# Optimization experiments

Measured on AMD Instinct MI355X. Metric: run time of the kernel, lower is better.

Reference implementation:

```python
import jax, jax.numpy as jnp
import numpy as np

B, T, F, D, H, L, DFF, G = 4, 2048, 512, 1024, 16, 2, 4096, 16
WSCALE = 0.03  # ~1/sqrt(D) so activations stay well-conditioned


def setup_inputs() -> dict:
    key = jax.random.key(0)
    ks = iter(jax.random.split(key, 24))

    def w(shape):
        return jax.random.normal(next(ks), shape, jnp.float32) * WSCALE

    return {
        "x": jax.random.normal(next(ks), (B, T, F), jnp.float32),
        "proj_w": w((D, F)), "proj_b": jnp.zeros((D,), jnp.float32),
        "wq": w((L, D, D)), "wk": w((L, D, D)), "wv": w((L, D, D)),
        "bq": jnp.zeros((L, D), jnp.float32), "bk": jnp.zeros((L, D), jnp.float32), "bv": jnp.zeros((L, D), jnp.float32),
        "wo": w((L, D, D)), "bo": jnp.zeros((L, D), jnp.float32),
        "ln1_g": jnp.ones((L, D), jnp.float32), "ln1_b": jnp.zeros((L, D), jnp.float32),
        "ln2_g": jnp.ones((L, D), jnp.float32), "ln2_b": jnp.zeros((L, D), jnp.float32),
        "w1": w((L, DFF, D)), "b1": jnp.zeros((L, DFF), jnp.float32),
        "w2": w((L, D, DFF)), "b2": jnp.zeros((L, D), jnp.float32),
        "hw1": w((G, D, D)), "hb1": jnp.zeros((G, D), jnp.float32),
        "hw2": w((G, 2, D)), "hb2": jnp.zeros((G, 2), jnp.float32),
        "nhead": H,
    }


def _ln(x, g, b, eps=1e-5):
    m = x.mean(-1, keepdims=True)
    v = ((x - m) ** 2).mean(-1, keepdims=True)
    return (x - m) * jax.lax.rsqrt(v + eps) * g + b


def _pe(t, d):
    # sinusoidal positional encoding, shape (t, d) (d even -> sin/cos interleave)
    pos = jnp.arange(t, dtype=jnp.float32)[:, None]
    div = jnp.exp(jnp.arange(0, d, 2, dtype=jnp.float32) * (-np.log(10000.0) / d))
    ph = pos * div
    return jnp.stack([jnp.sin(ph), jnp.cos(ph)], axis=-1).reshape(t, d)


def reference(x, proj_w, proj_b, wq, wk, wv, bq, bk, bv, wo, bo,
              ln1_g, ln1_b, ln2_g, ln2_b, w1, b1, w2, b2,
              hw1, hb1, hw2, hb2, nhead):
    Bx, Tx, _ = x.shape
    Dm = proj_w.shape[0]
    dh = Dm // nhead
    h = x @ proj_w.T + proj_b + _pe(Tx, Dm)  # (B,T,D)
    for l in range(wq.shape[0]):  # post-norm encoder layers
        q = (h @ wq[l].T + bq[l]).reshape(Bx, Tx, nhead, dh)
        k = (h @ wk[l].T + bk[l]).reshape(Bx, Tx, nhead, dh)
        v = (h @ wv[l].T + bv[l]).reshape(Bx, Tx, nhead, dh)
        # explicit (non-fused) attention path, as forced by need_weights=True
        scores = jnp.einsum('bthd,bshd->bhts', q, k) / jnp.sqrt(jnp.float32(dh))
        attn = jax.nn.softmax(scores, axis=-1)  # (B,H,T,T)
        ctx = jnp.einsum('bhts,bshd->bthd', attn, v).reshape(Bx, Tx, Dm)
        h = _ln(h + ctx @ wo[l].T + bo[l], ln1_g[l], ln1_b[l])
        ff = jax.nn.relu(h @ w1[l].T + b1[l]) @ w2[l].T + b2[l]
        h = _ln(h + ff, ln2_g[l], ln2_b[l])
    hl = h[:, -1, :]  # last-token pooling, (B,D)
    z = jax.nn.relu(jnp.einsum('bd,gkd->bgk', hl, hw1) + hb1)  # per-sector hidden
    logits = jnp.einsum('bgk,gok->bgo', z, hw2) + hb2           # (B,G,2)
    return jax.nn.softmax(logits, axis=-1)
```

## Files before the change

### kernel.cpp

```cpp
#include <hip/hip_runtime.h>
#include <hip/hip_bf16.h>
#include <cstdint>
#include <cstddef>


typedef __bf16 bf16_t;
typedef __attribute__((ext_vector_type(8))) __bf16 bf16x8;
typedef __attribute__((ext_vector_type(4))) __bf16 bf16x4;
typedef __attribute__((ext_vector_type(4))) float f32x4;
typedef __attribute__((ext_vector_type(16))) float f32x16;
typedef __attribute__((ext_vector_type(2))) unsigned u32x2;
typedef __attribute__((ext_vector_type(4))) unsigned u32x4;

#define DEV __device__ __forceinline__
#define AS1 __attribute__((address_space(1)))
#define AS3 __attribute__((address_space(3)))

DEV void gload_lds16(const void* g, void* l) {
  __builtin_amdgcn_global_load_lds((AS1 void*)(g), (AS3 void*)(l), 16, 0, 0);
}

DEV const char* swz_ptr(const void* base, int row, int colb) {
  return (const char*)base + row * 128 + ((((colb >> 4) ^ (row & 7))) << 4) +
         (colb & 15);
}

DEV unsigned cvtpk(float lo, float hi) {
  unsigned r;
  asm("v_cvt_pk_bf16_f32 %0, %1, %2" : "=v"(r) : "v"(lo), "v"(hi));
  return r;
}
DEV void swap32(unsigned& a, unsigned& b) {
  u32x2 r = __builtin_amdgcn_permlane32_swap(a, b, false, false);
  a = r[0];
  b = r[1];
}
DEV bf16x8 mkfrag(unsigned w0, unsigned w1, unsigned w2, unsigned w3) {
  u32x4 v = {w0, w1, w2, w3};
  return __builtin_bit_cast(bf16x8, v);
}

__global__ __launch_bounds__(256) void f2b_kernel(const float* __restrict__ s,
                                                  bf16_t* __restrict__ d, int n4) {
  const int i = blockIdx.x * 256 + threadIdx.x;
  if (i >= n4) return;
  const float4 v = *(const float4*)&s[(size_t)i * 4];
  bf16x4 o = {(bf16_t)v.x, (bf16_t)v.y, (bf16_t)v.z, (bf16_t)v.w};
  *(bf16x4*)&d[(size_t)i * 4] = o;
}

__global__ __launch_bounds__(256) void bcat_kernel(const float* __restrict__ bq,
                                                   const float* __restrict__ bk,
                                                   const float* __restrict__ bv,
                                                   float* __restrict__ out) {
  const int idx = blockIdx.x * 256 + threadIdx.x;
  const int l = idx / 3072, r = idx - l * 3072;
  const int p = r >> 10, i = r & 1023;
  const float* s = (p == 0) ? bq : ((p == 1) ? bk : bv);
  out[idx] = s[l * 1024 + i];
}

__global__ __launch_bounds__(256) void pe_kernel(float* __restrict__ pe) {
  const int idx = blockIdx.x * 256 + threadIdx.x;
  const int t = idx >> 9, i = idx & 511;
  const float dv = __expf((float)(2 * i) * -0.008994473019508785f);
  const float ph = (float)t * dv;
  pe[(size_t)t * 1024 + 2 * i] = sinf(ph);
  pe[(size_t)t * 1024 + 2 * i + 1] = cosf(ph);
}

template <int EPI, int BM, int BN>
__global__ __launch_bounds__(BM == 256 ? 512 : 256, 2) void gemm9(
    const bf16_t* __restrict__ A, const bf16_t* __restrict__ W,
    const float* __restrict__ bias, bf16_t* __restrict__ outb,
    float* __restrict__ outf, const float* __restrict__ res32,
    const float* __restrict__ pe, int M, int N, int K) {
  constexpr int T = (BM == 256) ? 512 : 256;
  constexpr int RPC = T / 8;
  constexpr int NA = (BM * 128) / (T * 16);
  constexpr int NB = (BN * 128) / (T * 16);
  constexpr int LPT = NA + NB;
  constexpr bool WIDE = (BM == 256 && BN == 256);
  constexpr int MF = WIDE ? 8 : 4;
  constexpr int ASZ = BM * 128;
  constexpr int BUFSZ = (BM + BN) * 128;
  __shared__ char smem[2][BUFSZ];
  const int tid = threadIdx.x, wv = tid >> 6, ln = tid & 63;
  const int nwg = gridDim.x * gridDim.y;
  int bid = blockIdx.y * gridDim.x + blockIdx.x;
  bid = (bid & 7) * (nwg >> 3) + (bid >> 3);
  const int m0 = (bid / gridDim.x) * BM, n0 = (bid % gridDim.x) * BN;
  const int wrow = WIDE ? (wv >> 2) * 128 : (wv >> 1) * 64;
  const int wcol = WIDE ? (wv & 3) * 64 : (wv & 1) * 64;
  f32x4 acc[MF][4] = {};

  const int tp = tid ^ ((tid >> 3) & 7);
  const int srow = tp >> 3, sc8 = (tp & 7) * 8;
  const bf16_t* pa[NA];
  const bf16_t* pb[NB];
#pragma unroll
  for (int u = 0; u < NA; ++u) pa[u] = A + (size_t)(m0 + u * RPC + srow) * K + sc8;
#pragma unroll
  for (int u = 0; u < NB; ++u) pb[u] = W + (size_t)(n0 + u * RPC + srow) * K + sc8;
  const int wvb = wv * 1024;

  auto stage = [&](int s) {
    char* bA = &smem[s][0] + wvb;
    char* bB = &smem[s][ASZ] + wvb;
#pragma unroll
    for (int u = 0; u < NA; ++u) {
      gload_lds16(pa[u], bA + u * (T * 16));
      pa[u] += 64;
    }
#pragma unroll
    for (int u = 0; u < NB; ++u) {
      gload_lds16(pb[u], bB + u * (T * 16));
      pb[u] += 64;
    }
  };

  auto wait_lpt = [&]() {
    if constexpr (LPT == 8)
      asm volatile("s_waitcnt vmcnt(8)" ::: "memory");
    else
      asm volatile("s_waitcnt vmcnt(6)" ::: "memory");
  };

  const int NK = K >> 6;
  stage(0);
  stage(1);
  wait_lpt();
  __builtin_amdgcn_s_barrier();

  for (int kt = 0; kt < NK; ++kt) {
    const char* bA = &smem[kt & 1][0];
    const char* bB = &smem[kt & 1][ASZ];
#pragma unroll
    for (int ks = 0; ks < 2; ++ks) {
      const int cb = ks * 64 + (ln >> 4) * 16;
      bf16x8 bF[4];
#pragma unroll
      for (int n = 0; n < 4; ++n) {
        const int lb = (wcol + n * 16 + (ln & 15)) * 128 + cb;
        bF[n] = *(const bf16x8*)(bB + (lb ^ (((lb >> 7) & 7) << 4)));
      }
#pragma unroll
      for (int mh = 0; mh < 2; ++mh) {
        bf16x8 aF[MF / 2];
#pragma unroll
        for (int m = 0; m < MF / 2; ++m) {
          const int lb = (wrow + (mh * (MF / 2) + m) * 16 + (ln & 15)) * 128 + cb;
          aF[m] = *(const bf16x8*)(bA + (lb ^ (((lb >> 7) & 7) << 4)));
        }
        __builtin_amdgcn_s_setprio(1);
#pragma unroll
        for (int m = 0; m < MF / 2; ++m)
#pragma unroll
          for (int n = 0; n < 4; ++n)
            acc[mh * (MF / 2) + m][n] = __builtin_amdgcn_mfma_f32_16x16x32_bf16(
                aF[m], bF[n], acc[mh * (MF / 2) + m][n], 0, 0, 0);
        __builtin_amdgcn_s_setprio(0);
      }
    }
    __builtin_amdgcn_s_barrier();
    if (kt + 2 < NK) {
      stage(kt & 1);
      wait_lpt();
    } else if (kt + 1 < NK) {
      asm volatile("s_waitcnt vmcnt(0)" ::: "memory");
    }
    __builtin_amdgcn_s_barrier();
    __builtin_amdgcn_sched_barrier(0);
  }

  const int rr = (ln >> 4) * 4, cc = ln & 15;
#pragma unroll
  for (int m = 0; m < MF; ++m) {
    const int rowb = m0 + wrow + m * 16 + rr;
#pragma unroll
    for (int n = 0; n < 4; ++n) {
      const int col = n0 + wcol + n * 16 + cc;
      const float bv = bias[col];
#pragma unroll
      for (int r = 0; r < 4; ++r) {
        const int row = rowb + r;
        float v = acc[m][n][r] + bv;
        const size_t o = (size_t)row * N + col;
        if constexpr (EPI == 1) {
          v = fmaxf(v, 0.f);
          outb[o] = (bf16_t)v;
        } else if constexpr (EPI == 2) {
          v += pe[(size_t)(row & 2047) * 1024 + col];
          outb[o] = (bf16_t)v;
          outf[o] = v;
        } else if constexpr (EPI == 3) {
          v += res32[o];
          outf[o] = v;
        } else {
          outb[o] = (bf16_t)v;
        }
      }
    }
  }
}

__global__ __launch_bounds__(256) void ln_kernel(const float* __restrict__ pre,
                                                 const float* __restrict__ g,
                                                 const float* __restrict__ b,
                                                 bf16_t* __restrict__ h16,
                                                 float* __restrict__ h32) {
  const int row = blockIdx.x, tid = threadIdx.x;
  const size_t base = (size_t)row * 1024 + tid * 4;
  const float4 v = *(const float4*)&pre[base];
  float s = v.x + v.y + v.z + v.w;
  float s2 = v.x * v.x + v.y * v.y + v.z * v.z + v.w * v.w;
#pragma unroll
  for (int m = 1; m < 64; m <<= 1) {
    s += __shfl_xor(s, m);
    s2 += __shfl_xor(s2, m);
  }
  __shared__ float ls[4], ls2[4];
  if ((tid & 63) == 0) {
    ls[tid >> 6] = s;
    ls2[tid >> 6] = s2;
  }
  __syncthreads();
  s = ls[0] + ls[1] + ls[2] + ls[3];
  s2 = ls2[0] + ls2[1] + ls2[2] + ls2[3];
  const float mean = s * (1.f / 1024.f);
  const float var = s2 * (1.f / 1024.f) - mean * mean;
  const float rs = rsqrtf(var + 1e-5f);
  const float4 gv = *(const float4*)&g[tid * 4];
  const float4 bv = *(const float4*)&b[tid * 4];
  const float o0 = (v.x - mean) * rs * gv.x + bv.x;
  const float o1 = (v.y - mean) * rs * gv.y + bv.y;
  const float o2 = (v.z - mean) * rs * gv.z + bv.z;
  const float o3 = (v.w - mean) * rs * gv.w + bv.w;
  bf16x4 ob = {(bf16_t)o0, (bf16_t)o1, (bf16_t)o2, (bf16_t)o3};
  *(bf16x4*)&h16[base] = ob;
  float4 of = {o0, o1, o2, o3};
  *(float4*)&h32[base] = of;
}

__global__ __launch_bounds__(256) void transpose_v(const bf16_t* __restrict__ v,
                                                   bf16_t* __restrict__ vt) {
  __shared__ bf16_t tile[64][80];
  const int bh = blockIdx.y, t0 = blockIdx.x * 64;
  const int tid = threadIdx.x;
  const int b = bh >> 4;
  const size_t vbase = ((size_t)(b * 2048 + t0)) * 3072 + (bh & 15) * 64;
#pragma unroll
  for (int p = 0; p < 2; ++p) {
    const int chunk = p * 256 + tid;
    const int tr = chunk >> 3, c8 = (chunk & 7) * 8;
    *(bf16x8*)&tile[tr][c8] = *(const bf16x8*)&v[vbase + (size_t)tr * 3072 + c8];
  }
  __syncthreads();
  const int d = tid >> 2, t8 = (tid & 3) * 16;
  bf16_t tmp[16];
#pragma unroll
  for (int j = 0; j < 16; ++j) tmp[j] = tile[t8 + j][d];
  const size_t obase = ((size_t)bh * 64 + d) * 2048 + t0 + t8;
  *(bf16x8*)&vt[obase] = *(bf16x8*)&tmp[0];
  *(bf16x8*)&vt[obase + 8] = *(bf16x8*)&tmp[8];
}

__global__ __launch_bounds__(256, 4) void attn_kernel(const bf16_t* __restrict__ qkv,
                                                      const bf16_t* __restrict__ vt,
                                                      bf16_t* __restrict__ ctx) {
  constexpr float SCL = 0.18033688011112042f;
  constexpr int QS = 3072;
  __shared__ bf16_t lK[2][64 * 64];
  __shared__ bf16_t lV[2][64 * 64];
  const int tid = threadIdx.x, wv = tid >> 6, ln = tid & 63;
  const int nwg = gridDim.x * gridDim.y;
  int bid = blockIdx.y * gridDim.x + blockIdx.x;
  bid = (bid & 7) * (nwg >> 3) + (bid >> 3);
  const int bh = bid / gridDim.x, b = bh >> 4, h = bh & 15;
  const int q0 = (bid % gridDim.x) * 128 + wv * 32;
  const int lq = ln & 31, hi = ln >> 5;
  const bf16_t* qp = qkv + (size_t)(b * 2048 + q0 + lq) * QS + h * 64 + hi * 8;
  bf16x8 qF[4];
#pragma unroll
  for (int kk = 0; kk < 4; ++kk) qF[kk] = *(const bf16x8*)(qp + kk * 16);
  f32x16 O0 = {}, O1 = {};
  float l_q = 0.f;
  const int sr = tid >> 3;
  const int scS = ((tid & 7) ^ ((tid >> 3) & 7)) * 8;
  const bf16_t* kp0 = qkv + 1024 + (size_t)(b * 2048 + sr) * QS + h * 64 + scS;
  const bf16_t* kp1 = kp0 + (size_t)32 * QS;
  const bf16_t* vp0 = vt + (size_t)bh * 64 * 2048 + (size_t)sr * 2048 + scS;
  const bf16_t* vp1 = vp0 + 32 * 2048;

  auto stage = [&](int bufi) {
    char* dk = (char*)&lK[bufi][0] + wv * 1024;
    char* dv = (char*)&lV[bufi][0] + wv * 1024;
    gload_lds16(kp0, dk);
    gload_lds16(kp1, dk + 4096);
    gload_lds16(vp0, dv);
    gload_lds16(vp1, dv + 4096);
    kp0 += (size_t)64 * QS;
    kp1 += (size_t)64 * QS;
    vp0 += 64;
    vp1 += 64;
  };

  stage(0);
  asm volatile("s_waitcnt vmcnt(0)" ::: "memory");
  __builtin_amdgcn_s_barrier();

  for (int st = 0; st < 32; ++st) {
    const int cur = st & 1;
    if (st + 1 < 32) stage(cur ^ 1);
#pragma unroll
    for (int sb = 0; sb < 2; ++sb) {
      f32x16 s = {};
      __builtin_amdgcn_s_setprio(1);
#pragma unroll
      for (int kk = 0; kk < 4; ++kk) {
        const bf16x8 kf =
            *(const bf16x8*)swz_ptr(&lK[cur][0], sb * 32 + lq, kk * 32 + hi * 16);
        s = __builtin_amdgcn_mfma_f32_32x32x16_bf16(kf, qF[kk], s, 0, 0, 0);
      }
      __builtin_amdgcn_s_setprio(0);
      float ra = 0.f, rb = 0.f;
#pragma unroll
      for (int i = 0; i < 8; ++i) {
        s[i] = exp2f(s[i] * SCL);
        ra += s[i];
        s[i + 8] = exp2f(s[i + 8] * SCL);
        rb += s[i + 8];
      }
      float rsum = ra + rb;
      rsum += __shfl_xor(rsum, 32);
      l_q += rsum;
      unsigned A = cvtpk(s[0], s[1]), Bq = cvtpk(s[2], s[3]);
      unsigned C = cvtpk(s[4], s[5]), Dq = cvtpk(s[6], s[7]);
      unsigned A2 = cvtpk(s[8], s[9]), B2 = cvtpk(s[10], s[11]);
      unsigned C2 = cvtpk(s[12], s[13]), D2 = cvtpk(s[14], s[15]);
      swap32(A, C);
      swap32(Bq, Dq);
      swap32(A2, C2);
      swap32(B2, D2);
      const bf16x8 f0 = mkfrag(A, Bq, C, Dq);
      const bf16x8 f1 = mkfrag(A2, B2, C2, D2);
      __builtin_amdgcn_s_setprio(1);
      const bf16x8 va = *(const bf16x8*)swz_ptr(&lV[cur][0], lq, sb * 64 + hi * 16);
      const bf16x8 vb =
          *(const bf16x8*)swz_ptr(&lV[cur][0], lq, sb * 64 + 32 + hi * 16);
      const bf16x8 vc =
          *(const bf16x8*)swz_ptr(&lV[cur][0], 32 + lq, sb * 64 + hi * 16);
      const bf16x8 vd =
          *(const bf16x8*)swz_ptr(&lV[cur][0], 32 + lq, sb * 64 + 32 + hi * 16);
      O0 = __builtin_amdgcn_mfma_f32_32x32x16_bf16(f0, va, O0, 0, 0, 0);
      O0 = __builtin_amdgcn_mfma_f32_32x32x16_bf16(f1, vb, O0, 0, 0, 0);
      O1 = __builtin_amdgcn_mfma_f32_32x32x16_bf16(f0, vc, O1, 0, 0, 0);
      O1 = __builtin_amdgcn_mfma_f32_32x32x16_bf16(f1, vd, O1, 0, 0, 0);
      __builtin_amdgcn_s_setprio(0);
    }
    asm volatile("s_waitcnt vmcnt(0)" ::: "memory");
    __builtin_amdgcn_s_barrier();
    __builtin_amdgcn_sched_barrier(0);
  }
  const float invl = 1.f / l_q;
  const size_t obase = ((size_t)(b * 2048 + q0)) * 1024 + h * 64 + lq;
#pragma unroll
  for (int r = 0; r < 16; ++r) {
    const int qr = (r & 3) + 8 * (r >> 2) + 4 * hi;
    const float iv = __shfl(invl, qr);
    ctx[obase + (size_t)qr * 1024] = (bf16_t)(O0[r] * iv);
    ctx[obase + (size_t)qr * 1024 + 32] = (bf16_t)(O1[r] * iv);
  }
}

__global__ __launch_bounds__(256) void head_z(const float* __restrict__ h32,
                                              const float* __restrict__ hw1,
                                              const float* __restrict__ hb1,
                                              float* __restrict__ z) {
  const int g = blockIdx.x, slab = blockIdx.y;
  const int wv = threadIdx.x >> 6, ln = threadIdx.x & 63;
  float4 hl[4][4];
#pragma unroll
  for (int b = 0; b < 4; ++b)
#pragma unroll
    for (int c = 0; c < 4; ++c)
      hl[b][c] = *(const float4*)&h32[((size_t)b * 2048 + 2047) * 1024 + c * 256 + ln * 4];
  const int k0 = slab * 64 + wv * 16;
  for (int kk = 0; kk < 16; ++kk) {
    const int kq = k0 + kk;
    const float* wrow = hw1 + ((size_t)g * 1024 + kq) * 1024;
    float p[4] = {0, 0, 0, 0};
#pragma unroll
    for (int c = 0; c < 4; ++c) {
      const float4 w4 = *(const float4*)&wrow[c * 256 + ln * 4];
#pragma unroll
      for (int b = 0; b < 4; ++b)
        p[b] += w4.x * hl[b][c].x + w4.y * hl[b][c].y + w4.z * hl[b][c].z +
                w4.w * hl[b][c].w;
    }
#pragma unroll
    for (int m = 1; m < 64; m <<= 1)
#pragma unroll
      for (int b = 0; b < 4; ++b) p[b] += __shfl_xor(p[b], m);
    if (ln == 0) {
#pragma unroll
      for (int b = 0; b < 4; ++b)
        z[((size_t)b * 16 + g) * 1024 + kq] = fmaxf(p[b] + hb1[g * 1024 + kq], 0.f);
    }
  }
}

__global__ __launch_bounds__(64) void head_logits(const float* __restrict__ z,
                                                  const float* __restrict__ hw2,
                                                  const float* __restrict__ hb2,
                                                  float* __restrict__ out) {
  const int b = blockIdx.x, g = blockIdx.y, ln = threadIdx.x;
  const float* zr = z + ((size_t)b * 16 + g) * 1024;
  const float* w0 = hw2 + (size_t)g * 2048;
  const float* w1 = w0 + 1024;
  float p0 = 0.f, p1 = 0.f;
#pragma unroll
  for (int c = 0; c < 4; ++c) {
    const float4 zv = *(const float4*)&zr[c * 256 + ln * 4];
    const float4 a0 = *(const float4*)&w0[c * 256 + ln * 4];
    const float4 a1 = *(const float4*)&w1[c * 256 + ln * 4];
    p0 += zv.x * a0.x + zv.y * a0.y + zv.z * a0.z + zv.w * a0.w;
    p1 += zv.x * a1.x + zv.y * a1.y + zv.z * a1.z + zv.w * a1.w;
  }
#pragma unroll
  for (int m = 1; m < 64; m <<= 1) {
    p0 += __shfl_xor(p0, m);
    p1 += __shfl_xor(p1, m);
  }
  if (ln == 0) {
    const float l0 = p0 + hb2[g * 2], l1 = p1 + hb2[g * 2 + 1];
    const float mx = fmaxf(l0, l1);
    const float e0 = expf(l0 - mx), e1 = expf(l1 - mx);
    const float inv = 1.f / (e0 + e1);
    out[(size_t)b * 32 + g * 2] = e0 * inv;
    out[(size_t)b * 32 + g * 2 + 1] = e1 * inv;
  }
}

extern "C" void kernel_launch(void* const* d_in, const int* in_sizes, int n_in,
                              void* d_out, int out_size, void* d_ws, size_t ws_size,
                              hipStream_t stream) {
  const float* x = (const float*)d_in[0];
  const float* proj_w = (const float*)d_in[1];
  const float* proj_b = (const float*)d_in[2];
  const float* wq = (const float*)d_in[3];
  const float* wk = (const float*)d_in[4];
  const float* wvv = (const float*)d_in[5];
  const float* bq = (const float*)d_in[6];
  const float* bk = (const float*)d_in[7];
  const float* bv = (const float*)d_in[8];
  const float* wo = (const float*)d_in[9];
  const float* bo = (const float*)d_in[10];
  const float* ln1_g = (const float*)d_in[11];
  const float* ln1_b = (const float*)d_in[12];
  const float* ln2_g = (const float*)d_in[13];
  const float* ln2_b = (const float*)d_in[14];
  const float* w1 = (const float*)d_in[15];
  const float* b1 = (const float*)d_in[16];
  const float* w2 = (const float*)d_in[17];
  const float* b2 = (const float*)d_in[18];
  const float* hw1 = (const float*)d_in[19];
  const float* hb1 = (const float*)d_in[20];
  const float* hw2 = (const float*)d_in[21];
  const float* hb2 = (const float*)d_in[22];
  float* out = (float*)d_out;
  char* ws = (char*)d_ws;

  size_t o = 0;
  auto take = [&](size_t bytes) { size_t r = o; o += bytes; return r; };
  const size_t o_wqkv = take(12582912);
  const size_t o_wo = take(4194304);
  const size_t o_w1 = take(16777216);
  const size_t o_w2 = take(16777216);
  const size_t o_pw = take(1048576);
  const size_t o_h16 = take(16777216);
  const size_t o_h32 = take(33554432);
  const size_t o_pre = take(33554432);
  const size_t o_r4 = take(67108864);
  const size_t o_r5 = take(16777216);
  const size_t o_z = take(262144);
  const size_t o_bqkv = take(24576);

  bf16_t* wqkv16 = (bf16_t*)(ws + o_wqkv);
  bf16_t* wo16 = (bf16_t*)(ws + o_wo);
  bf16_t* w1_16 = (bf16_t*)(ws + o_w1);
  bf16_t* w2_16 = (bf16_t*)(ws + o_w2);
  bf16_t* pw16 = (bf16_t*)(ws + o_pw);
  bf16_t* h16 = (bf16_t*)(ws + o_h16);
  float* h32 = (float*)(ws + o_h32);
  float* pre32 = (float*)(ws + o_pre);
  bf16_t* qkv16 = (bf16_t*)(ws + o_r4);
  bf16_t* vT16 = (bf16_t*)(ws + o_r4 + 50331648);
  bf16_t* ff1 = (bf16_t*)(ws + o_r4);
  bf16_t* x16 = (bf16_t*)(ws + o_r5);
  float* pe32 = (float*)(ws + o_r5 + 8388608);
  bf16_t* ctx16 = (bf16_t*)(ws + o_r5);
  float* zbuf = (float*)(ws + o_z);
  float* bqkv = (float*)(ws + o_bqkv);

  f2b_kernel<<<4096, 256, 0, stream>>>(x, x16, 1048576);
  f2b_kernel<<<512, 256, 0, stream>>>(proj_w, pw16, 131072);
  for (int l = 0; l < 2; ++l) {
    f2b_kernel<<<1024, 256, 0, stream>>>(wq + (size_t)l * 1048576,
                                         wqkv16 + (size_t)(l * 3 + 0) * 1048576, 262144);
    f2b_kernel<<<1024, 256, 0, stream>>>(wk + (size_t)l * 1048576,
                                         wqkv16 + (size_t)(l * 3 + 1) * 1048576, 262144);
    f2b_kernel<<<1024, 256, 0, stream>>>(wvv + (size_t)l * 1048576,
                                         wqkv16 + (size_t)(l * 3 + 2) * 1048576, 262144);
  }
  f2b_kernel<<<2048, 256, 0, stream>>>(wo, wo16, 524288);
  f2b_kernel<<<8192, 256, 0, stream>>>(w1, w1_16, 2097152);
  f2b_kernel<<<8192, 256, 0, stream>>>(w2, w2_16, 2097152);
  bcat_kernel<<<24, 256, 0, stream>>>(bq, bk, bv, bqkv);
  pe_kernel<<<4096, 256, 0, stream>>>(pe32);

  gemm9<2, 128, 128><<<dim3(8, 64), 256, 0, stream>>>(x16, pw16, proj_b, h16, h32,
                                                      nullptr, pe32, 8192, 1024, 512);

  for (int l = 0; l < 2; ++l) {
    const bf16_t* wqkv_l = wqkv16 + (size_t)l * 3145728;
    const bf16_t* wo_l = wo16 + (size_t)l * 1048576;
    const bf16_t* w1_l = w1_16 + (size_t)l * 4194304;
    const bf16_t* w2_l = w2_16 + (size_t)l * 4194304;

    gemm9<0, 256, 128><<<dim3(24, 32), 512, 0, stream>>>(h16, wqkv_l, bqkv + l * 3072,
                                                         qkv16, nullptr, nullptr,
                                                         nullptr, 8192, 3072, 1024);
    transpose_v<<<dim3(32, 64), 256, 0, stream>>>(qkv16 + 2048, vT16);
    attn_kernel<<<dim3(16, 64), 256, 0, stream>>>(qkv16, vT16, ctx16);
    gemm9<3, 128, 128><<<dim3(8, 64), 256, 0, stream>>>(ctx16, wo_l, bo + l * 1024,
                                                        nullptr, pre32, h32, nullptr,
                                                        8192, 1024, 1024);
    ln_kernel<<<8192, 256, 0, stream>>>(pre32, ln1_g + l * 1024, ln1_b + l * 1024, h16,
                                        h32);
    gemm9<1, 256, 256><<<dim3(16, 32), 512, 0, stream>>>(h16, w1_l, b1 + l * 4096, ff1,
                                                         nullptr, nullptr, nullptr,
                                                         8192, 4096, 1024);
    gemm9<3, 128, 128><<<dim3(8, 64), 256, 0, stream>>>(ff1, w2_l, b2 + l * 1024,
                                                        nullptr, pre32, h32, nullptr,
                                                        8192, 1024, 4096);
    ln_kernel<<<8192, 256, 0, stream>>>(pre32, ln2_g + l * 1024, ln2_b + l * 1024, h16,
                                        h32);
  }

  head_z<<<dim3(16, 16), 256, 0, stream>>>(h32, hw1, hb1, zbuf);
  head_logits<<<dim3(4, 16), 64, 0, stream>>>(zbuf, hw2, hb2, out);
}
```

Measured before the change: 865.7 us.

## Drop fp32 residual stream, fuse weight conversions, prescale Q in attention

The fp32 hidden and pre-norm buffers are removed. Residual adds and layernorm now read and write bf16, which halves epilogue and LN memory traffic. The many per-tensor f32-to-bf16 conversion launches are merged into one kernel, and the softmax scale is folded into Q when it loads, so the per-score multiply is gone. The cost is lower precision in the residual stream, which accumulates rounding error across layers.

```diff
diff --git a/kernel.cpp b/kernel.cpp
--- a/kernel.cpp
+++ b/kernel.cpp
@@ -40,13 +40,47 @@
   return __builtin_bit_cast(bf16x8, v);
 }
 
-__global__ __launch_bounds__(256) void f2b_kernel(const float* __restrict__ s,
-                                                  bf16_t* __restrict__ d, int n4) {
-  const int i = blockIdx.x * 256 + threadIdx.x;
-  if (i >= n4) return;
-  const float4 v = *(const float4*)&s[(size_t)i * 4];
+__global__ __launch_bounds__(256) void convert_all(
+    const float* __restrict__ x, const float* __restrict__ proj_w,
+    const float* __restrict__ wq, const float* __restrict__ wk,
+    const float* __restrict__ wvv, const float* __restrict__ wo,
+    const float* __restrict__ w1, const float* __restrict__ w2,
+    bf16_t* __restrict__ x16, bf16_t* __restrict__ pw16,
+    bf16_t* __restrict__ wqkv16, bf16_t* __restrict__ wo16,
+    bf16_t* __restrict__ w1_16, bf16_t* __restrict__ w2_16) {
+  const int blk = blockIdx.x, tid = threadIdx.x;
+  const float* s;
+  bf16_t* d;
+  if (blk < 4096) {
+    s = x + (size_t)blk * 1024;
+    d = x16 + (size_t)blk * 1024;
+  } else if (blk < 4608) {
+    const int q = blk - 4096;
+    s = proj_w + (size_t)q * 1024;
+    d = pw16 + (size_t)q * 1024;
+  } else if (blk < 10752) {
+    const int q = blk - 4608;
+    const int sub = q >> 10, off = q & 1023;
+    const int l = sub / 3, p = sub - l * 3;
+    const float* base = (p == 0) ? wq : ((p == 1) ? wk : wvv);
+    s = base + (size_t)l * 1048576 + (size_t)off * 1024;
+    d = wqkv16 + (size_t)sub * 1048576 + (size_t)off * 1024;
+  } else if (blk < 12800) {
+    const int q = blk - 10752;
+    s = wo + (size_t)q * 1024;
+    d = wo16 + (size_t)q * 1024;
+  } else if (blk < 20992) {
+    const int q = blk - 12800;
+    s = w1 + (size_t)q * 1024;
+    d = w1_16 + (size_t)q * 1024;
+  } else {
+    const int q = blk - 20992;
+    s = w2 + (size_t)q * 1024;
+    d = w2_16 + (size_t)q * 1024;
+  }
+  const float4 v = *(const float4*)&s[tid * 4];
   bf16x4 o = {(bf16_t)v.x, (bf16_t)v.y, (bf16_t)v.z, (bf16_t)v.w};
-  *(bf16x4*)&d[(size_t)i * 4] = o;
+  *(bf16x4*)&d[tid * 4] = o;
 }
 
 __global__ __launch_bounds__(256) void bcat_kernel(const float* __restrict__ bq,
@@ -73,8 +107,8 @@
 __global__ __launch_bounds__(BM == 256 ? 512 : 256, 2) void gemm9(
     const bf16_t* __restrict__ A, const bf16_t* __restrict__ W,
     const float* __restrict__ bias, bf16_t* __restrict__ outb,
-    float* __restrict__ outf, const float* __restrict__ res32,
-    const float* __restrict__ pe, int M, int N, int K) {
+    const bf16_t* __restrict__ res16, const float* __restrict__ pe, int M,
+    int N, int K) {
   constexpr int T = (BM == 256) ? 512 : 256;
   constexpr int RPC = T / 8;
   constexpr int NA = (BM * 128) / (T * 16);
@@ -188,32 +222,28 @@
         const size_t o = (size_t)row * N + col;
         if constexpr (EPI == 1) {
           v = fmaxf(v, 0.f);
-          outb[o] = (bf16_t)v;
         } else if constexpr (EPI == 2) {
           v += pe[(size_t)(row & 2047) * 1024 + col];
-          outb[o] = (bf16_t)v;
-          outf[o] = v;
         } else if constexpr (EPI == 3) {
-          v += res32[o];
-          outf[o] = v;
-        } else {
-          outb[o] = (bf16_t)v;
+          v += (float)res16[o];
         }
+        outb[o] = (bf16_t)v;
       }
     }
   }
 }
 
-__global__ __launch_bounds__(256) void ln_kernel(const float* __restrict__ pre,
+__global__ __launch_bounds__(256) void ln_kernel(const bf16_t* __restrict__ pre,
                                                  const float* __restrict__ g,
                                                  const float* __restrict__ b,
-                                                 bf16_t* __restrict__ h16,
-                                                 float* __restrict__ h32) {
+                                                 bf16_t* __restrict__ h16) {
   const int row = blockIdx.x, tid = threadIdx.x;
   const size_t base = (size_t)row * 1024 + tid * 4;
-  const float4 v = *(const float4*)&pre[base];
-  float s = v.x + v.y + v.z + v.w;
-  float s2 = v.x * v.x + v.y * v.y + v.z * v.z + v.w * v.w;
+  const bf16x4 pv = *(const bf16x4*)&pre[base];
+  const float v0 = (float)pv[0], v1 = (float)pv[1], v2 = (float)pv[2],
+              v3 = (float)pv[3];
+  float s = v0 + v1 + v2 + v3;
+  float s2 = v0 * v0 + v1 * v1 + v2 * v2 + v3 * v3;
 #pragma unroll
   for (int m = 1; m < 64; m <<= 1) {
     s += __shfl_xor(s, m);
@@ -232,14 +262,11 @@
   const float rs = rsqrtf(var + 1e-5f);
   const float4 gv = *(const float4*)&g[tid * 4];
   const float4 bv = *(const float4*)&b[tid * 4];
-  const float o0 = (v.x - mean) * rs * gv.x + bv.x;
-  const float o1 = (v.y - mean) * rs * gv.y + bv.y;
-  const float o2 = (v.z - mean) * rs * gv.z + bv.z;
-  const float o3 = (v.w - mean) * rs * gv.w + bv.w;
-  bf16x4 ob = {(bf16_t)o0, (bf16_t)o1, (bf16_t)o2, (bf16_t)o3};
+  bf16x4 ob = {(bf16_t)((v0 - mean) * rs * gv.x + bv.x),
+               (bf16_t)((v1 - mean) * rs * gv.y + bv.y),
+               (bf16_t)((v2 - mean) * rs * gv.z + bv.z),
+               (bf16_t)((v3 - mean) * rs * gv.w + bv.w)};
   *(bf16x4*)&h16[base] = ob;
-  float4 of = {o0, o1, o2, o3};
-  *(float4*)&h32[base] = of;
 }
 
 __global__ __launch_bounds__(256) void transpose_v(const bf16_t* __restrict__ v,
@@ -282,7 +309,14 @@
   const bf16_t* qp = qkv + (size_t)(b * 2048 + q0 + lq) * QS + h * 64 + hi * 8;
   bf16x8 qF[4];
 #pragma unroll
-  for (int kk = 0; kk < 4; ++kk) qF[kk] = *(const bf16x8*)(qp + kk * 16);
+  for (int kk = 0; kk < 4; ++kk) {
+    const bf16x8 raw = *(const bf16x8*)(qp + kk * 16);
+    unsigned w[4];
+#pragma unroll
+    for (int j = 0; j < 4; ++j)
+      w[j] = cvtpk((float)raw[2 * j] * SCL, (float)raw[2 * j + 1] * SCL);
+    qF[kk] = mkfrag(w[0], w[1], w[2], w[3]);
+  }
   f32x16 O0 = {}, O1 = {};
   float l_q = 0.f;
   const int sr = tid >> 3;
@@ -326,9 +360,9 @@
       float ra = 0.f, rb = 0.f;
 #pragma unroll
       for (int i = 0; i < 8; ++i) {
-        s[i] = exp2f(s[i] * SCL);
+        s[i] = exp2f(s[i]);
         ra += s[i];
-        s[i + 8] = exp2f(s[i + 8] * SCL);
+        s[i + 8] = exp2f(s[i + 8]);
         rb += s[i + 8];
       }
       float rsum = ra + rb;
@@ -373,7 +407,7 @@
   }
 }
 
-__global__ __launch_bounds__(256) void head_z(const float* __restrict__ h32,
+__global__ __launch_bounds__(256) void head_z(const bf16_t* __restrict__ h16,
                                               const float* __restrict__ hw1,
                                               const float* __restrict__ hb1,
                                               float* __restrict__ z) {
@@ -383,8 +417,11 @@
 #pragma unroll
   for (int b = 0; b < 4; ++b)
 #pragma unroll
-    for (int c = 0; c < 4; ++c)
-      hl[b][c] = *(const float4*)&h32[((size_t)b * 2048 + 2047) * 1024 + c * 256 + ln * 4];
+    for (int c = 0; c < 4; ++c) {
+      const bf16x4 hv = *(const bf16x4*)&h16[((size_t)b * 2048 + 2047) * 1024 +
+                                             c * 256 + ln * 4];
+      hl[b][c] = make_float4((float)hv[0], (float)hv[1], (float)hv[2], (float)hv[3]);
+    }
   const int k0 = slab * 64 + wv * 16;
   for (int kk = 0; kk < 16; ++kk) {
     const int kq = k0 + kk;
@@ -479,8 +516,7 @@
   const size_t o_w2 = take(16777216);
   const size_t o_pw = take(1048576);
   const size_t o_h16 = take(16777216);
-  const size_t o_h32 = take(33554432);
-  const size_t o_pre = take(33554432);
+  const size_t o_pre = take(16777216);
   const size_t o_r4 = take(67108864);
   const size_t o_r5 = take(16777216);
   const size_t o_z = take(262144);
@@ -492,8 +528,7 @@
   bf16_t* w2_16 = (bf16_t*)(ws + o_w2);
   bf16_t* pw16 = (bf16_t*)(ws + o_pw);
   bf16_t* h16 = (bf16_t*)(ws + o_h16);
-  float* h32 = (float*)(ws + o_h32);
-  float* pre32 = (float*)(ws + o_pre);
+  bf16_t* pre16 = (bf16_t*)(ws + o_pre);
   bf16_t* qkv16 = (bf16_t*)(ws + o_r4);
   bf16_t* vT16 = (bf16_t*)(ws + o_r4 + 50331648);
   bf16_t* ff1 = (bf16_t*)(ws + o_r4);
@@ -503,24 +538,13 @@
   float* zbuf = (float*)(ws + o_z);
   float* bqkv = (float*)(ws + o_bqkv);
 
-  f2b_kernel<<<4096, 256, 0, stream>>>(x, x16, 1048576);
-  f2b_kernel<<<512, 256, 0, stream>>>(proj_w, pw16, 131072);
-  for (int l = 0; l < 2; ++l) {
-    f2b_kernel<<<1024, 256, 0, stream>>>(wq + (size_t)l * 1048576,
-                                         wqkv16 + (size_t)(l * 3 + 0) * 1048576, 262144);
-    f2b_kernel<<<1024, 256, 0, stream>>>(wk + (size_t)l * 1048576,
-                                         wqkv16 + (size_t)(l * 3 + 1) * 1048576, 262144);
-    f2b_kernel<<<1024, 256, 0, stream>>>(wvv + (size_t)l * 1048576,
-                                         wqkv16 + (size_t)(l * 3 + 2) * 1048576, 262144);
-  }
-  f2b_kernel<<<2048, 256, 0, stream>>>(wo, wo16, 524288);
-  f2b_kernel<<<8192, 256, 0, stream>>>(w1, w1_16, 2097152);
-  f2b_kernel<<<8192, 256, 0, stream>>>(w2, w2_16, 2097152);
+  convert_all<<<29184, 256, 0, stream>>>(x, proj_w, wq, wk, wvv, wo, w1, w2, x16,
+                                         pw16, wqkv16, wo16, w1_16, w2_16);
   bcat_kernel<<<24, 256, 0, stream>>>(bq, bk, bv, bqkv);
   pe_kernel<<<4096, 256, 0, stream>>>(pe32);
 
-  gemm9<2, 128, 128><<<dim3(8, 64), 256, 0, stream>>>(x16, pw16, proj_b, h16, h32,
-                                                      nullptr, pe32, 8192, 1024, 512);
+  gemm9<2, 128, 128><<<dim3(8, 64), 256, 0, stream>>>(x16, pw16, proj_b, h16, nullptr,
+                                                      pe32, 8192, 1024, 512);
 
   for (int l = 0; l < 2; ++l) {
     const bf16_t* wqkv_l = wqkv16 + (size_t)l * 3145728;
@@ -529,25 +553,25 @@
     const bf16_t* w2_l = w2_16 + (size_t)l * 4194304;
 
     gemm9<0, 256, 128><<<dim3(24, 32), 512, 0, stream>>>(h16, wqkv_l, bqkv + l * 3072,
-                                                         qkv16, nullptr, nullptr,
-                                                         nullptr, 8192, 3072, 1024);
+                                                         qkv16, nullptr, nullptr, 8192,
+                                                         3072, 1024);
     transpose_v<<<dim3(32, 64), 256, 0, stream>>>(qkv16 + 2048, vT16);
     attn_kernel<<<dim3(16, 64), 256, 0, stream>>>(qkv16, vT16, ctx16);
     gemm9<3, 128, 128><<<dim3(8, 64), 256, 0, stream>>>(ctx16, wo_l, bo + l * 1024,
-                                                        nullptr, pre32, h32, nullptr,
-                                                        8192, 1024, 1024);
-    ln_kernel<<<8192, 256, 0, stream>>>(pre32, ln1_g + l * 1024, ln1_b + l * 1024, h16,
-                                        h32);
+                                                        pre16, h16, nullptr, 8192,
+                                                        1024, 1024);
+    ln_kernel<<<8192, 256, 0, stream>>>(pre16, ln1_g + l * 1024, ln1_b + l * 1024,
+                                        h16);
     gemm9<1, 256, 256><<<dim3(16, 32), 512, 0, stream>>>(h16, w1_l, b1 + l * 4096, ff1,
-                                                         nullptr, nullptr, nullptr,
-                                                         8192, 4096, 1024);
+                                                         nullptr, nullptr, 8192, 4096,
+                                                         1024);
     gemm9<3, 128, 128><<<dim3(8, 64), 256, 0, stream>>>(ff1, w2_l, b2 + l * 1024,
-                                                        nullptr, pre32, h32, nullptr,
-                                                        8192, 1024, 4096);
-    ln_kernel<<<8192, 256, 0, stream>>>(pre32, ln2_g + l * 1024, ln2_b + l * 1024, h16,
-                                        h32);
-  }
-
-  head_z<<<dim3(16, 16), 256, 0, stream>>>(h32, hw1, hb1, zbuf);
+                                                        pre16, h16, nullptr, 8192,
+                                                        1024, 4096);
+    ln_kernel<<<8192, 256, 0, stream>>>(pre16, ln2_g + l * 1024, ln2_b + l * 1024,
+                                        h16);
+  }
+
+  head_z<<<dim3(16, 16), 256, 0, stream>>>(h16, hw1, hb1, zbuf);
   head_logits<<<dim3(4, 16), 64, 0, stream>>>(zbuf, hw2, hb2, out);
 }
```

Result: faster. 817.6 us (-5.6%).
